# Kernel tuning notes

Measured on AMD Instinct MI355X. Metric: run time of the kernel, lower is better.

## Reference

```python
import jax, jax.numpy as jnp
import numpy as np
import math

C = 512
NUM_HEADS = 4
GROUPS = 32  # group_count(512, 32)
EPS = 1e-5


def group_norm(x, gamma, beta):
    # x: [b, c, h, w]; normalize over (c//GROUPS, h, w) per group
    b, c, h, w = x.shape
    xg = x.reshape(b, GROUPS, -1)
    mu = jnp.mean(xg, axis=-1, keepdims=True)
    var = jnp.var(xg, axis=-1, keepdims=True)
    xn = ((xg - mu) * jax.lax.rsqrt(var + EPS)).reshape(b, c, h, w)
    return xn * gamma[None, :, None, None] + beta[None, :, None, None]


def setup_inputs() -> dict:
    key = jax.random.key(0)
    ks = jax.random.split(key, 5)
    b, h, w = 2, 64, 64
    x = jax.random.normal(ks[0], (b, C, h, w), dtype=jnp.float32)
    gn_w = jnp.ones((C,), dtype=jnp.float32)
    gn_b = jnp.zeros((C,), dtype=jnp.float32)
    s_qkv = 1.0 / math.sqrt(C)
    w_qkv = jax.random.uniform(ks[1], (3 * C, C), jnp.float32, -s_qkv, s_qkv)
    b_qkv = jax.random.uniform(ks[2], (3 * C,), jnp.float32, -s_qkv, s_qkv)
    w_proj = jax.random.uniform(ks[3], (C, C), jnp.float32, -s_qkv, s_qkv)
    b_proj = jax.random.uniform(ks[4], (C,), jnp.float32, -s_qkv, s_qkv)
    return {"x": x, "gn_w": gn_w, "gn_b": gn_b, "w_qkv": w_qkv,
            "b_qkv": b_qkv, "w_proj": w_proj, "b_proj": b_proj}


def reference(x, gn_w, gn_b, w_qkv, b_qkv, w_proj, b_proj):
    b, c, h, w = x.shape
    L = h * w
    nh = NUM_HEADS
    hd = c // nh
    residual = x
    xn = group_norm(x, gn_w, gn_b).reshape(b, c, L)
    # Conv1d with kernel_size=1 == channelwise linear: [b, 3c, L]
    qkv = jnp.einsum('bcl,oc->bol', xn, w_qkv) + b_qkv[None, :, None]
    q, k, v = jnp.split(qkv, 3, axis=1)
    q = q.reshape(b, nh, hd, L)
    k = k.reshape(b, nh, hd, L)
    v = v.reshape(b, nh, hd, L)
    scores = jnp.einsum('bncd,bnce->bnde', q, k) / math.sqrt(hd)
    attn = jax.nn.softmax(scores, axis=-1)
    out = jnp.einsum('bnde,bnce->bncd', attn, v).reshape(b, c, L)
    out = jnp.einsum('bcl,oc->bol', out, w_proj) + b_proj[None, :, None]
    return out.reshape(b, c, h, w) + residual
```

## Files before the change

kernel.cpp:

```cpp
#include <hip/hip_runtime.h>
#include <math.h>

typedef __bf16 bf16;
typedef __bf16 bf16x8 __attribute__((ext_vector_type(8)));
typedef __bf16 bf16x4 __attribute__((ext_vector_type(4)));
typedef float f32x4 __attribute__((ext_vector_type(4)));

#define QSCALE (0.08838834764831845f * 1.4426950408889634f)

__device__ __forceinline__ void gll16(const bf16* g, bf16* l) {
    __builtin_amdgcn_global_load_lds((const __attribute__((address_space(1))) void*)g,
                                     (__attribute__((address_space(3))) void*)l, 16, 0, 0);
}

__global__ void k_pre(const float* __restrict__ wqkv, const float* __restrict__ wproj,
                      const float* __restrict__ x,
                      bf16* __restrict__ wqkv_b, bf16* __restrict__ wproj_b,
                      float* __restrict__ part) {
    int blk = blockIdx.x;
    if (blk < 1024) {
        int i = blk * 256 + threadIdx.x;
        const int n1 = (1536 * 512) / 4;
        float4 v;
        bf16* dst;
        if (i < n1) { v = ((const float4*)wqkv)[i];      dst = wqkv_b + (size_t)i * 4; }
        else        { v = ((const float4*)wproj)[i - n1]; dst = wproj_b + (size_t)(i - n1) * 4; }
        bf16x4 o;
        o[0] = (bf16)v.x; o[1] = (bf16)v.y; o[2] = (bf16)v.z; o[3] = (bf16)v.w;
        *(bf16x4*)dst = o;
        return;
    }
    int b2 = blk - 1024;
    int grp = b2 >> 2, p = b2 & 3;
    const float4* src = (const float4*)(x + (size_t)grp * 65536 + (size_t)p * 16384);
    float s = 0.f, ss = 0.f;
    for (int it = 0; it < 16; ++it) {
        float4 v = src[threadIdx.x + it * 256];
        s  += v.x + v.y + v.z + v.w;
        ss += v.x * v.x + v.y * v.y + v.z * v.z + v.w * v.w;
    }
    for (int off = 32; off; off >>= 1) { s += __shfl_down(s, off); ss += __shfl_down(ss, off); }
    __shared__ float rs[4], rss[4];
    int wave = threadIdx.x >> 6;
    if ((threadIdx.x & 63) == 0) { rs[wave] = s; rss[wave] = ss; }
    __syncthreads();
    if (threadIdx.x == 0) {
        part[(grp * 4 + p) * 2]     = rs[0] + rs[1] + rs[2] + rs[3];
        part[(grp * 4 + p) * 2 + 1] = rss[0] + rss[1] + rss[2] + rss[3];
    }
}

__global__ __launch_bounds__(256) void k_gn_norm_t(const float* __restrict__ x, const float* __restrict__ gw,
                                                   const float* __restrict__ gb, const float* __restrict__ part,
                                                   bf16* __restrict__ xn_t) {
    __shared__ float sX[64 * 69];
    __shared__ float sMean[4], sRstd[4];
    int b = blockIdx.z, c0 = blockIdx.y * 64, l0 = blockIdx.x * 64;
    int t = threadIdx.x;
    if (t < 4) {
        int g = b * 32 + (c0 >> 4) + t;
        float S = 0.f, SS = 0.f;
        for (int p = 0; p < 4; ++p) { S += part[(g * 4 + p) * 2]; SS += part[(g * 4 + p) * 2 + 1]; }
        float mean = S * (1.f / 65536.f);
        float var  = SS * (1.f / 65536.f) - mean * mean;
        sMean[t] = mean;
        sRstd[t] = rsqrtf(var + 1e-5f);
    }
    __syncthreads();
    int cr = t >> 4, lq = t & 15;
    const float* xp = x + ((size_t)(b * 512 + c0)) * 4096 + l0;
    for (int i = 0; i < 4; ++i) {
        int c = cr + i * 16;
        int cg = c0 + c;
        float mean = sMean[c >> 4], rstd = sRstd[c >> 4];
        float ga = gw[cg] * rstd;
        float be = gb[cg] - mean * ga;
        float4 v = *(const float4*)(xp + (size_t)c * 4096 + lq * 4);
        float* d = &sX[c * 69 + lq * 4];
        d[0] = v.x * ga + be; d[1] = v.y * ga + be; d[2] = v.z * ga + be; d[3] = v.w * ga + be;
    }
    __syncthreads();
    int lr = t >> 3, cp = t & 7;
    bf16* dst = xn_t + ((size_t)b * 4096 + l0) * 512 + c0;
    for (int i = 0; i < 2; ++i) {
        int l = lr + i * 32;
        bf16x8 o;
        for (int j = 0; j < 8; ++j) o[j] = (bf16)sX[(cp * 8 + j) * 69 + l];
        *(bf16x8*)(dst + (size_t)l * 512 + cp * 8) = o;
    }
}

__global__ __launch_bounds__(256, 3) void k_gemm_qkv(
    const bf16* __restrict__ A, const bf16* __restrict__ W, const float* __restrict__ bias,
    bf16* __restrict__ qkT, bf16* __restrict__ vb) {
    __shared__ bf16 smem[17408];
    int linear = blockIdx.x + 12 * blockIdx.y + 384 * blockIdx.z;
    int swz = (linear & 7) * 96 + (linear >> 3);
    int n0 = (swz % 12) * 128;
    int m0 = ((swz / 12) % 32) * 128;
    int bz = swz / 384;
    int tid = threadIdx.x, lane = tid & 63, wave = tid >> 6;
    int lo = lane & 15, quad = lane >> 4;
    int lr = lane >> 3, ls = lane & 7;
    int mw = (wave >> 1) * 64, nw = (wave & 1) * 64;
    const bf16* aptr[4]; int adst[4];
    const bf16* bptr[4]; int bdst[4];
    for (int i = 0; i < 4; ++i) {
        int r0 = wave * 32 + i * 8;
        int row = r0 + lr;
        aptr[i] = A + (size_t)bz * (4096 * 512) + (size_t)(m0 + row) * 512 + ((ls ^ (row & 7)) * 8);
        adst[i] = r0 * 64;
        bptr[i] = W + (size_t)(n0 + row) * 512 + ((ls ^ (row & 7)) * 8);
        bdst[i] = 8192 + r0 * 64;
    }
    f32x4 acc[4][4] = {};
    for (int step = 0; step < 8; ++step) {
        __syncthreads();
        for (int i = 0; i < 4; ++i) {
            gll16(aptr[i], &smem[adst[i]]); aptr[i] += 64;
            gll16(bptr[i], &smem[bdst[i]]); bptr[i] += 64;
        }
        __syncthreads();
        const bf16* sA = smem;
        const bf16* sB = smem + 8192;
        for (int kk = 0; kk < 2; ++kk) {
            bf16x8 af[4], bfr[4];
            int sw = ((kk * 4 + quad) ^ (lo & 7)) * 8;
            for (int t = 0; t < 4; ++t) af[t]  = *(const bf16x8*)&sA[(mw + t * 16 + lo) * 64 + sw];
            for (int t = 0; t < 4; ++t) bfr[t] = *(const bf16x8*)&sB[(nw + t * 16 + lo) * 64 + sw];
            for (int mt = 0; mt < 4; ++mt)
                for (int nt = 0; nt < 4; ++nt)
                    acc[mt][nt] = __builtin_amdgcn_mfma_f32_16x16x32_bf16(af[mt], bfr[nt], acc[mt][nt], 0, 0, 0);
        }
    }
    __syncthreads();
    bf16* sT = smem;
    bool isv = (n0 >= 1024);
    float sc = (n0 < 512) ? QSCALE : 1.f;
    for (int mt = 0; mt < 4; ++mt)
        for (int nt = 0; nt < 4; ++nt) {
            int c = nw + nt * 16 + lo;
            float bv = bias[n0 + c];
            for (int r = 0; r < 4; ++r) {
                int l = mw + mt * 16 + quad * 4 + r;
                float v = (acc[mt][nt][r] + bv) * sc;
                if (isv) sT[c * 136 + l] = (bf16)v;
                else     sT[l * 136 + c] = (bf16)v;
            }
        }
    __syncthreads();
    int row = tid >> 1, hh = tid & 1;
    if (isv) {
        bf16* dst = vb + (size_t)bz * (512 * 4096) + (size_t)(n0 - 1024 + row) * 4096 + m0;
        for (int j = 0; j < 8; ++j) {
            int ch = hh + j * 2;
            *(bf16x8*)(dst + ch * 8) = *(const bf16x8*)&sT[row * 136 + ch * 8];
        }
    } else {
        bf16* dst = qkT + (size_t)bz * (4096 * 1024) + (size_t)(m0 + row) * 1024 + n0;
        for (int j = 0; j < 8; ++j) {
            int ch = hh + j * 2;
            *(bf16x8*)(dst + ch * 8) = *(const bf16x8*)&sT[row * 136 + ch * 8];
        }
    }
}

__global__ __launch_bounds__(256, 3) void k_gemm_proj(
    const bf16* __restrict__ W, const bf16* __restrict__ Bm,
    const float* __restrict__ bias_m,
    float* __restrict__ outf, const float* __restrict__ resid) {
    constexpr int BUF = (64 + 128) * 64;
    __shared__ bf16 smem[2 * BUF];
    int bz = blockIdx.z;
    int m0 = blockIdx.y * 64, n0 = blockIdx.x * 128;
    int tid = threadIdx.x, lane = tid & 63, wave = tid >> 6;
    int lo = lane & 15, quad = lane >> 4;
    int lr = lane >> 3, ls = lane & 7;
    int mw = (wave >> 1) * 32, nw = (wave & 1) * 64;
    const bf16* aptr[2]; int adst[2];
    for (int i = 0; i < 2; ++i) {
        int r0 = wave * 16 + i * 8;
        int row = r0 + lr;
        aptr[i] = W + (size_t)(m0 + row) * 512 + ((ls ^ (row & 7)) * 8);
        adst[i] = r0 * 64;
    }
    const bf16* bptr[4]; int bdst[4];
    for (int i = 0; i < 4; ++i) {
        int r0 = wave * 32 + i * 8;
        int row = r0 + lr;
        bptr[i] = Bm + (size_t)bz * (4096 * 512) + (size_t)(n0 + row) * 512 + ((ls ^ (row & 7)) * 8);
        bdst[i] = 64 * 64 + r0 * 64;
    }
    f32x4 acc[2][4] = {};
    for (int i = 0; i < 2; ++i) { gll16(aptr[i], &smem[adst[i]]); aptr[i] += 64; }
    for (int i = 0; i < 4; ++i) { gll16(bptr[i], &smem[bdst[i]]); bptr[i] += 64; }
    for (int step = 0; step < 8; ++step) {
        int cur = step & 1;
        __syncthreads();
        if (step < 7) {
            bf16* nb = &smem[(cur ^ 1) * BUF];
            for (int i = 0; i < 2; ++i) { gll16(aptr[i], nb + adst[i]); aptr[i] += 64; }
            for (int i = 0; i < 4; ++i) { gll16(bptr[i], nb + bdst[i]); bptr[i] += 64; }
        }
        const bf16* sA = &smem[cur * BUF];
        const bf16* sB = sA + 64 * 64;
        for (int kk = 0; kk < 2; ++kk) {
            bf16x8 af[2], bfr[4];
            int sw = ((kk * 4 + quad) ^ (lo & 7)) * 8;
            for (int t = 0; t < 2; ++t) af[t]  = *(const bf16x8*)&sA[(mw + t * 16 + lo) * 64 + sw];
            for (int t = 0; t < 4; ++t) bfr[t] = *(const bf16x8*)&sB[(nw + t * 16 + lo) * 64 + sw];
            for (int mt = 0; mt < 2; ++mt)
                for (int nt = 0; nt < 4; ++nt)
                    acc[mt][nt] = __builtin_amdgcn_mfma_f32_16x16x32_bf16(af[mt], bfr[nt], acc[mt][nt], 0, 0, 0);
        }
    }
    for (int mt = 0; mt < 2; ++mt) {
        int rowb = m0 + mw + mt * 16 + quad * 4;
        for (int nt = 0; nt < 4; ++nt) {
            int col = n0 + nw + nt * 16 + lo;
            for (int r = 0; r < 4; ++r) {
                int row = rowb + r;
                size_t idx = (size_t)bz * (512 * 4096) + (size_t)row * 4096 + col;
                outf[idx] = acc[mt][nt][r] + bias_m[row] + resid[idx];
            }
        }
    }
}

__global__ __launch_bounds__(512, 2) void k_attn(const bf16* __restrict__ qkT, const bf16* __restrict__ vmat,
                                                 bf16* __restrict__ attnT) {
    __shared__ __align__(16) char smem[104448];
    bf16* sE = (bf16*)smem;
    float* sStat = (float*)(smem + 102400);
    int bidx = blockIdx.x;
    int bh = bidx & 7;
    int bb = bh >> 2, h = bh & 3;
    int l0 = (bidx >> 3) * 128;
    int tid = threadIdx.x, lane = tid & 63, wave = tid >> 6;
    int lo = lane & 15, quad = lane >> 4;
    int a = wave & 3, b2 = wave >> 2;
    int lr16 = lane >> 4, ls16 = lane & 15;
    int lr8 = lane >> 3, ls8 = lane & 7;
    const bf16* qbase = qkT + ((size_t)bb * 4096 + l0) * 1024 + h * 128;
    const bf16* kbase = qkT + (size_t)bb * 4096 * 1024 + 512 + h * 128;
    const bf16* vbase = vmat + (size_t)(bb * 512 + h * 128) * 4096;
    for (int i = 0; i < 4; ++i) {
        int r0 = wave * 16 + i * 4;
        int row = r0 + lr16;
        gll16(qbase + (size_t)row * 1024 + ((ls16 ^ (row & 15)) * 8), sE + r0 * 128);
    }
    __syncthreads();
    bf16x8 qf[2][4];
    for (int nt = 0; nt < 2; ++nt) {
        int row = a * 32 + nt * 16 + lo;
        for (int kk = 0; kk < 4; ++kk)
            qf[nt][kk] = *(const bf16x8*)&sE[row * 128 + (((kk * 4 + quad) ^ lo) * 8)];
    }
    __syncthreads();
    const bf16* kptr[2]; int kdst[2];
    const bf16* vptr[2]; int vdst[2];
    for (int i = 0; i < 2; ++i) {
        int r0 = wave * 8 + i * 4;
        int row = r0 + lr16;
        kptr[i] = kbase + (size_t)row * 1024 + ((ls16 ^ (row & 15)) * 8);
        kdst[i] = r0 * 128;
        int s0 = wave * 16 + i * 8;
        int srow = s0 + lr8;
        vptr[i] = vbase + (size_t)srow * 4096 + ((ls8 ^ (srow & 7)) * 8);
        vdst[i] = s0 * 64;
    }
    bf16* sPe = (bf16*)(smem + 65536) + wave * 1280;
    float l_r[2];
    l_r[0] = l_r[1] = 0.f;
    f32x4 oacc[8][2] = {};
    for (int i = 0; i < 2; ++i) { gll16(kptr[i], sE + kdst[i]); kptr[i] += (size_t)64 * 1024; }
    for (int i = 0; i < 2; ++i) { gll16(vptr[i], sE + 16384 + vdst[i]); vptr[i] += 64; }
    for (int it = 0; it < 64; ++it) {
        int cur = it & 1;
        __syncthreads();
        if (it < 63) {
            bf16* nk = sE + (cur ^ 1) * 8192;
            bf16* nv = sE + 16384 + (cur ^ 1) * 8192;
            for (int i = 0; i < 2; ++i) { gll16(kptr[i], nk + kdst[i]); kptr[i] += (size_t)64 * 1024; }
            for (int i = 0; i < 2; ++i) { gll16(vptr[i], nv + vdst[i]); vptr[i] += 64; }
        }
        const bf16* sK = sE + cur * 8192;
        const bf16* sV = sE + 16384 + cur * 8192;
        f32x4 s[2][2];
        for (int mt = 0; mt < 2; ++mt) {
            int krow = b2 * 32 + mt * 16 + lo;
            bf16x8 kf[4];
            for (int kk = 0; kk < 4; ++kk)
                kf[kk] = *(const bf16x8*)&sK[krow * 128 + (((kk * 4 + quad) ^ lo) * 8)];
            for (int nt = 0; nt < 2; ++nt) {
                f32x4 acc = {};
                for (int kk = 0; kk < 4; ++kk)
                    acc = __builtin_amdgcn_mfma_f32_16x16x32_bf16(kf[kk], qf[nt][kk], acc, 0, 0, 0);
                s[mt][nt] = acc;
            }
        }
        for (int nt = 0; nt < 2; ++nt) {
            float sm = 0.f;
            for (int mt = 0; mt < 2; ++mt) {
                bf16x4 pk;
                for (int r = 0; r < 4; ++r) {
                    float pv = __builtin_amdgcn_exp2f(s[mt][nt][r]);
                    sm += pv;
                    pk[r] = (bf16)pv;
                }
                *(bf16x4*)&sPe[(nt * 16 + lo) * 40 + mt * 16 + quad * 4] = pk;
            }
            l_r[nt] += sm;
        }
        bf16x8 pf[2];
        for (int nt = 0; nt < 2; ++nt)
            pf[nt] = *(const bf16x8*)&sPe[(nt * 16 + lo) * 40 + quad * 8];
        for (int mt2 = 0; mt2 < 8; ++mt2) {
            bf16x8 vf = *(const bf16x8*)&sV[(mt2 * 16 + lo) * 64 + (((b2 * 4 + quad) ^ (lo & 7)) * 8)];
            for (int nt = 0; nt < 2; ++nt)
                oacc[mt2][nt] = __builtin_amdgcn_mfma_f32_16x16x32_bf16(vf, pf[nt], oacc[mt2][nt], 0, 0, 0);
        }
    }
    for (int nt = 0; nt < 2; ++nt) {
        l_r[nt] += __shfl_xor(l_r[nt], 16);
        l_r[nt] += __shfl_xor(l_r[nt], 32);
    }
    __syncthreads();
    if (quad == 0) {
        for (int nt = 0; nt < 2; ++nt) {
            int qb = a * 32 + nt * 16 + lo;
            sStat[qb * 2 + b2] = l_r[nt];
        }
    }
    __syncthreads();
    float inv[2];
    for (int nt = 0; nt < 2; ++nt) {
        int qb = a * 32 + nt * 16 + lo;
        inv[nt] = 1.f / (sStat[qb * 2] + sStat[qb * 2 + 1]);
    }
    float* sOm = (float*)smem;
    bf16* sOut = (bf16*)(smem + 67584);
    if (b2 == 1) {
        for (int mt2 = 0; mt2 < 8; ++mt2)
            for (int nt = 0; nt < 2; ++nt)
                for (int r = 0; r < 4; ++r) {
                    int vc = mt2 * 16 + quad * 4 + r;
                    sOm[a * 4224 + vc * 33 + nt * 16 + lo] = oacc[mt2][nt][r];
                }
    }
    __syncthreads();
    if (b2 == 0) {
        for (int mt2 = 0; mt2 < 8; ++mt2)
            for (int nt = 0; nt < 2; ++nt)
                for (int r = 0; r < 4; ++r) {
                    int vc = mt2 * 16 + quad * 4 + r;
                    float v = (oacc[mt2][nt][r] + sOm[a * 4224 + vc * 33 + nt * 16 + lo]) * inv[nt];
                    sOut[(a * 32 + nt * 16 + lo) * 136 + vc] = (bf16)v;
                }
    }
    __syncthreads();
    bf16* dst = attnT + ((size_t)bb * 4096 + l0) * 512 + h * 128;
    for (int i = 0; i < 4; ++i) {
        int row = (tid >> 4) + i * 32;
        int chunk = tid & 15;
        bf16x8 v = *(const bf16x8*)&sOut[row * 136 + chunk * 8];
        *(bf16x8*)(dst + (size_t)row * 512 + chunk * 8) = v;
    }
}

extern "C" void kernel_launch(void* const* d_in, const int* in_sizes, int n_in,
                              void* d_out, int out_size, void* d_ws, size_t ws_size,
                              hipStream_t stream) {
    const float* x      = (const float*)d_in[0];
    const float* gn_w   = (const float*)d_in[1];
    const float* gn_b   = (const float*)d_in[2];
    const float* w_qkv  = (const float*)d_in[3];
    const float* b_qkv  = (const float*)d_in[4];
    const float* w_proj = (const float*)d_in[5];
    const float* b_proj = (const float*)d_in[6];
    float* out = (float*)d_out;
    char* ws = (char*)d_ws;
    bf16* wqkv_b  = (bf16*)(ws + 0);
    bf16* wproj_b = (bf16*)(ws + 1572864);
    bf16* xn_t    = (bf16*)(ws + 2097152);
    bf16* qkT     = (bf16*)(ws + 10485760);
    bf16* vb      = (bf16*)(ws + 27262976);
    bf16* attnT   = (bf16*)(ws + 35651584);
    float* part   = (float*)(ws + 44040192);

    k_pre<<<1280, 256, 0, stream>>>(w_qkv, w_proj, x, wqkv_b, wproj_b, part);
    k_gn_norm_t<<<dim3(64, 8, 2), 256, 0, stream>>>(x, gn_w, gn_b, part, xn_t);
    k_gemm_qkv<<<dim3(12, 32, 2), 256, 0, stream>>>(xn_t, wqkv_b, b_qkv, qkT, vb);
    k_attn<<<256, 512, 0, stream>>>(qkT, vb, attnT);
    k_gemm_proj<<<dim3(32, 8, 2), 256, 0, stream>>>(wproj_b, attnT, b_proj, out, x);
}
```

Measured before the change: 186.8 us.

## Restructure attention tiles: 128-key blocks, 64-query waves, 4-way key split

The attention kernel now processes 128 keys per iteration (32 iterations instead of 64), with each wave holding 64 query rows and the key dimension split four ways across waves. The larger per-wave tile is meant to raise MFMA work per LDS load and halve barrier count, and s_setprio hints are added around the MFMA bursts. In exchange it uses 160KB of shared memory, which likely limits occupancy to one block per CU despite launch bounds of 2, raises register pressure (oacc grows to 8x4), and needs a multi-stage cross-wave reduction at the end.

```diff
diff --git a/kernel.cpp b/kernel.cpp
--- a/kernel.cpp
+++ b/kernel.cpp
@@ -229,133 +229,152 @@
 
 __global__ __launch_bounds__(512, 2) void k_attn(const bf16* __restrict__ qkT, const bf16* __restrict__ vmat,
                                                  bf16* __restrict__ attnT) {
-    __shared__ __align__(16) char smem[104448];
+    __shared__ __align__(16) char smem[163840];
     bf16* sE = (bf16*)smem;
-    float* sStat = (float*)(smem + 102400);
     int bidx = blockIdx.x;
     int bh = bidx & 7;
     int bb = bh >> 2, h = bh & 3;
     int l0 = (bidx >> 3) * 128;
     int tid = threadIdx.x, lane = tid & 63, wave = tid >> 6;
     int lo = lane & 15, quad = lane >> 4;
-    int a = wave & 3, b2 = wave >> 2;
-    int lr16 = lane >> 4, ls16 = lane & 15;
-    int lr8 = lane >> 3, ls8 = lane & 7;
+    int a = wave & 1, b2 = wave >> 1;
     const bf16* qbase = qkT + ((size_t)bb * 4096 + l0) * 1024 + h * 128;
     const bf16* kbase = qkT + (size_t)bb * 4096 * 1024 + 512 + h * 128;
     const bf16* vbase = vmat + (size_t)(bb * 512 + h * 128) * 4096;
     for (int i = 0; i < 4; ++i) {
         int r0 = wave * 16 + i * 4;
-        int row = r0 + lr16;
-        gll16(qbase + (size_t)row * 1024 + ((ls16 ^ (row & 15)) * 8), sE + r0 * 128);
-    }
-    __syncthreads();
-    bf16x8 qf[2][4];
-    for (int nt = 0; nt < 2; ++nt) {
-        int row = a * 32 + nt * 16 + lo;
+        int row = r0 + quad;
+        gll16(qbase + (size_t)row * 1024 + ((lo ^ (row & 15)) * 8), sE + r0 * 128);
+    }
+    __syncthreads();
+    bf16x8 qf[4][4];
+    for (int nt = 0; nt < 4; ++nt) {
+        int row = a * 64 + nt * 16 + lo;
         for (int kk = 0; kk < 4; ++kk)
             qf[nt][kk] = *(const bf16x8*)&sE[row * 128 + (((kk * 4 + quad) ^ lo) * 8)];
     }
     __syncthreads();
-    const bf16* kptr[2]; int kdst[2];
-    const bf16* vptr[2]; int vdst[2];
-    for (int i = 0; i < 2; ++i) {
-        int r0 = wave * 8 + i * 4;
-        int row = r0 + lr16;
-        kptr[i] = kbase + (size_t)row * 1024 + ((ls16 ^ (row & 15)) * 8);
+    const bf16* kp[4]; int kdst[4];
+    const bf16* vp[4]; int vdst[4];
+    for (int i = 0; i < 4; ++i) {
+        int r0 = wave * 16 + i * 4;
+        int row = r0 + quad;
+        kp[i] = kbase + (size_t)row * 1024 + ((lo ^ (row & 15)) * 8);
         kdst[i] = r0 * 128;
-        int s0 = wave * 16 + i * 8;
-        int srow = s0 + lr8;
-        vptr[i] = vbase + (size_t)srow * 4096 + ((ls8 ^ (srow & 7)) * 8);
-        vdst[i] = s0 * 64;
-    }
-    bf16* sPe = (bf16*)(smem + 65536) + wave * 1280;
-    float l_r[2];
-    l_r[0] = l_r[1] = 0.f;
-    f32x4 oacc[8][2] = {};
-    for (int i = 0; i < 2; ++i) { gll16(kptr[i], sE + kdst[i]); kptr[i] += (size_t)64 * 1024; }
-    for (int i = 0; i < 2; ++i) { gll16(vptr[i], sE + 16384 + vdst[i]); vptr[i] += 64; }
-    for (int it = 0; it < 64; ++it) {
+        vp[i] = vbase + (size_t)row * 4096 + ((lo ^ (row & 15)) * 8);
+        vdst[i] = 32768 + r0 * 128;
+    }
+    char* sPb = smem + 131072 + a * 16384;
+    float l_r[4] = {};
+    f32x4 oacc[8][4] = {};
+    for (int i = 0; i < 4; ++i) { gll16(kp[i], sE + kdst[i]); kp[i] += 131072; }
+    for (int i = 0; i < 4; ++i) { gll16(vp[i], sE + vdst[i]); vp[i] += 128; }
+    for (int it = 0; it < 32; ++it) {
         int cur = it & 1;
         __syncthreads();
-        if (it < 63) {
-            bf16* nk = sE + (cur ^ 1) * 8192;
-            bf16* nv = sE + 16384 + (cur ^ 1) * 8192;
-            for (int i = 0; i < 2; ++i) { gll16(kptr[i], nk + kdst[i]); kptr[i] += (size_t)64 * 1024; }
-            for (int i = 0; i < 2; ++i) { gll16(vptr[i], nv + vdst[i]); vptr[i] += 64; }
-        }
-        const bf16* sK = sE + cur * 8192;
-        const bf16* sV = sE + 16384 + cur * 8192;
-        f32x4 s[2][2];
+        if (it < 31) {
+            int nb = (cur ^ 1) * 16384;
+            for (int i = 0; i < 4; ++i) { gll16(kp[i], sE + nb + kdst[i]); kp[i] += 131072; }
+            for (int i = 0; i < 4; ++i) { gll16(vp[i], sE + nb + vdst[i]); vp[i] += 128; }
+        }
+        const bf16* sK = sE + cur * 16384;
+        const bf16* sV = sE + 32768 + cur * 16384;
+        bf16x8 kf[2][4];
         for (int mt = 0; mt < 2; ++mt) {
             int krow = b2 * 32 + mt * 16 + lo;
-            bf16x8 kf[4];
             for (int kk = 0; kk < 4; ++kk)
-                kf[kk] = *(const bf16x8*)&sK[krow * 128 + (((kk * 4 + quad) ^ lo) * 8)];
-            for (int nt = 0; nt < 2; ++nt) {
-                f32x4 acc = {};
-                for (int kk = 0; kk < 4; ++kk)
-                    acc = __builtin_amdgcn_mfma_f32_16x16x32_bf16(kf[kk], qf[nt][kk], acc, 0, 0, 0);
-                s[mt][nt] = acc;
-            }
-        }
-        for (int nt = 0; nt < 2; ++nt) {
+                kf[mt][kk] = *(const bf16x8*)&sK[krow * 128 + (((kk * 4 + quad) ^ lo) * 8)];
+        }
+        for (int nt = 0; nt < 4; ++nt) {
+            f32x4 s0 = {}, s1 = {};
+            __builtin_amdgcn_s_setprio(1);
+            for (int kk = 0; kk < 4; ++kk)
+                s0 = __builtin_amdgcn_mfma_f32_16x16x32_bf16(kf[0][kk], qf[nt][kk], s0, 0, 0, 0);
+            for (int kk = 0; kk < 4; ++kk)
+                s1 = __builtin_amdgcn_mfma_f32_16x16x32_bf16(kf[1][kk], qf[nt][kk], s1, 0, 0, 0);
+            __builtin_amdgcn_s_setprio(0);
             float sm = 0.f;
-            for (int mt = 0; mt < 2; ++mt) {
+            int qrow = (nt * 16 + lo) * 256;
+            {
                 bf16x4 pk;
                 for (int r = 0; r < 4; ++r) {
-                    float pv = __builtin_amdgcn_exp2f(s[mt][nt][r]);
-                    sm += pv;
-                    pk[r] = (bf16)pv;
+                    float pv = __builtin_amdgcn_exp2f(s0[r]);
+                    sm += pv; pk[r] = (bf16)pv;
                 }
-                *(bf16x4*)&sPe[(nt * 16 + lo) * 40 + mt * 16 + quad * 4] = pk;
+                *(bf16x4*)&sPb[qrow + ((((b2 << 2) + (quad >> 1)) ^ lo) << 4) + ((quad & 1) << 3)] = pk;
+            }
+            {
+                bf16x4 pk;
+                for (int r = 0; r < 4; ++r) {
+                    float pv = __builtin_amdgcn_exp2f(s1[r]);
+                    sm += pv; pk[r] = (bf16)pv;
+                }
+                *(bf16x4*)&sPb[qrow + ((((b2 << 2) + 2 + (quad >> 1)) ^ lo) << 4) + ((quad & 1) << 3)] = pk;
             }
             l_r[nt] += sm;
         }
-        bf16x8 pf[2];
-        for (int nt = 0; nt < 2; ++nt)
-            pf[nt] = *(const bf16x8*)&sPe[(nt * 16 + lo) * 40 + quad * 8];
+        bf16x8 pf[4];
+        for (int nt = 0; nt < 4; ++nt)
+            pf[nt] = *(const bf16x8*)&sPb[(nt * 16 + lo) * 256 + ((((b2 << 2) + quad) ^ lo) << 4)];
+        __builtin_amdgcn_s_setprio(1);
         for (int mt2 = 0; mt2 < 8; ++mt2) {
-            bf16x8 vf = *(const bf16x8*)&sV[(mt2 * 16 + lo) * 64 + (((b2 * 4 + quad) ^ (lo & 7)) * 8)];
-            for (int nt = 0; nt < 2; ++nt)
+            bf16x8 vf = *(const bf16x8*)&sV[(mt2 * 16 + lo) * 128 + ((((b2 << 2) + quad) ^ lo) * 8)];
+            for (int nt = 0; nt < 4; ++nt)
                 oacc[mt2][nt] = __builtin_amdgcn_mfma_f32_16x16x32_bf16(vf, pf[nt], oacc[mt2][nt], 0, 0, 0);
         }
-    }
-    for (int nt = 0; nt < 2; ++nt) {
+        __builtin_amdgcn_s_setprio(0);
+    }
+    for (int nt = 0; nt < 4; ++nt) {
         l_r[nt] += __shfl_xor(l_r[nt], 16);
         l_r[nt] += __shfl_xor(l_r[nt], 32);
     }
     __syncthreads();
-    if (quad == 0) {
-        for (int nt = 0; nt < 2; ++nt) {
-            int qb = a * 32 + nt * 16 + lo;
-            sStat[qb * 2 + b2] = l_r[nt];
-        }
-    }
-    __syncthreads();
-    float inv[2];
-    for (int nt = 0; nt < 2; ++nt) {
-        int qb = a * 32 + nt * 16 + lo;
-        inv[nt] = 1.f / (sStat[qb * 2] + sStat[qb * 2 + 1]);
-    }
-    float* sOm = (float*)smem;
-    bf16* sOut = (bf16*)(smem + 67584);
-    if (b2 == 1) {
+    float* sStat = (float*)(smem + 139264);
+    if (quad == 0)
+        for (int nt = 0; nt < 4; ++nt)
+            sStat[(a * 64 + nt * 16 + lo) * 4 + b2] = l_r[nt];
+    __syncthreads();
+    float* sOmA = (float*)smem;
+    float* sOmB = (float*)(smem + 69632);
+    float inv[4];
+    if (b2 == 0)
+        for (int nt = 0; nt < 4; ++nt) {
+            const float* st = &sStat[(a * 64 + nt * 16 + lo) * 4];
+            inv[nt] = 1.f / (st[0] + st[1] + st[2] + st[3]);
+        }
+    if (b2 == 1 || b2 == 3) {
+        float* dm = (b2 == 1 ? sOmA : sOmB) + a * 8704;
         for (int mt2 = 0; mt2 < 8; ++mt2)
-            for (int nt = 0; nt < 2; ++nt)
+            for (int nt = 0; nt < 4; ++nt)
+                for (int r = 0; r < 4; ++r)
+                    dm[(mt2 * 16 + quad * 4 + r) * 68 + nt * 16 + lo] = oacc[mt2][nt][r];
+    }
+    __syncthreads();
+    if (b2 == 0 || b2 == 2) {
+        const float* sm2 = (b2 == 0 ? sOmA : sOmB) + a * 8704;
+        for (int mt2 = 0; mt2 < 8; ++mt2)
+            for (int nt = 0; nt < 4; ++nt)
+                for (int r = 0; r < 4; ++r)
+                    oacc[mt2][nt][r] += sm2[(mt2 * 16 + quad * 4 + r) * 68 + nt * 16 + lo];
+    }
+    __syncthreads();
+    if (b2 == 2) {
+        float* dm = sOmA + a * 8704;
+        for (int mt2 = 0; mt2 < 8; ++mt2)
+            for (int nt = 0; nt < 4; ++nt)
+                for (int r = 0; r < 4; ++r)
+                    dm[(mt2 * 16 + quad * 4 + r) * 68 + nt * 16 + lo] = oacc[mt2][nt][r];
+    }
+    __syncthreads();
+    bf16* sOut = (bf16*)(smem + 69632);
+    if (b2 == 0) {
+        const float* sm2 = sOmA + a * 8704;
+        for (int mt2 = 0; mt2 < 8; ++mt2)
+            for (int nt = 0; nt < 4; ++nt)
                 for (int r = 0; r < 4; ++r) {
                     int vc = mt2 * 16 + quad * 4 + r;
-                    sOm[a * 4224 + vc * 33 + nt * 16 + lo] = oacc[mt2][nt][r];
-                }
-    }
-    __syncthreads();
-    if (b2 == 0) {
-        for (int mt2 = 0; mt2 < 8; ++mt2)
-            for (int nt = 0; nt < 2; ++nt)
-                for (int r = 0; r < 4; ++r) {
-                    int vc = mt2 * 16 + quad * 4 + r;
-                    float v = (oacc[mt2][nt][r] + sOm[a * 4224 + vc * 33 + nt * 16 + lo]) * inv[nt];
-                    sOut[(a * 32 + nt * 16 + lo) * 136 + vc] = (bf16)v;
+                    float v = (oacc[mt2][nt][r] + sm2[vc * 68 + nt * 16 + lo]) * inv[nt];
+                    sOut[(a * 64 + nt * 16 + lo) * 136 + vc] = (bf16)v;
                 }
     }
     __syncthreads();
```

New measurement: 256.3 us. 37.2% more time.

## Double the attention key tile to 128 and add MFMA priority hints

Applied to the files above, without the earlier changes.

The attention kernel now processes 128 keys per iteration instead of 64. That halves the loop trip count and the number of block barriers, and K/V tiles are loaded with four async LDS loads per thread. Shared memory grows to 160KB, the P-tile layout is changed to a 128-byte swizzled row per query, and s_setprio brackets are placed around the MFMA sections. The cost is much larger LDS use, which with launch_bounds(512,2) can limit residency to one block per CU, plus more registers held per iteration.

```diff
diff --git a/kernel.cpp b/kernel.cpp
--- a/kernel.cpp
+++ b/kernel.cpp
@@ -229,9 +229,8 @@
 
 __global__ __launch_bounds__(512, 2) void k_attn(const bf16* __restrict__ qkT, const bf16* __restrict__ vmat,
                                                  bf16* __restrict__ attnT) {
-    __shared__ __align__(16) char smem[104448];
+    __shared__ __align__(16) char smem[163840];
     bf16* sE = (bf16*)smem;
-    float* sStat = (float*)(smem + 102400);
     int bidx = blockIdx.x;
     int bh = bidx & 7;
     int bb = bh >> 2, h = bh & 3;
@@ -239,15 +238,13 @@
     int tid = threadIdx.x, lane = tid & 63, wave = tid >> 6;
     int lo = lane & 15, quad = lane >> 4;
     int a = wave & 3, b2 = wave >> 2;
-    int lr16 = lane >> 4, ls16 = lane & 15;
-    int lr8 = lane >> 3, ls8 = lane & 7;
     const bf16* qbase = qkT + ((size_t)bb * 4096 + l0) * 1024 + h * 128;
     const bf16* kbase = qkT + (size_t)bb * 4096 * 1024 + 512 + h * 128;
     const bf16* vbase = vmat + (size_t)(bb * 512 + h * 128) * 4096;
     for (int i = 0; i < 4; ++i) {
         int r0 = wave * 16 + i * 4;
-        int row = r0 + lr16;
-        gll16(qbase + (size_t)row * 1024 + ((ls16 ^ (row & 15)) * 8), sE + r0 * 128);
+        int row = r0 + quad;
+        gll16(qbase + (size_t)row * 1024 + ((lo ^ (row & 15)) * 8), sE + r0 * 128);
     }
     __syncthreads();
     bf16x8 qf[2][4];
@@ -257,75 +254,74 @@
             qf[nt][kk] = *(const bf16x8*)&sE[row * 128 + (((kk * 4 + quad) ^ lo) * 8)];
     }
     __syncthreads();
-    const bf16* kptr[2]; int kdst[2];
-    const bf16* vptr[2]; int vdst[2];
-    for (int i = 0; i < 2; ++i) {
-        int r0 = wave * 8 + i * 4;
-        int row = r0 + lr16;
-        kptr[i] = kbase + (size_t)row * 1024 + ((ls16 ^ (row & 15)) * 8);
+    const bf16* kp[4]; int kdst[4];
+    const bf16* vp[4]; int vdst[4];
+    for (int i = 0; i < 4; ++i) {
+        int r0 = wave * 16 + i * 4;
+        int row = r0 + quad;
+        kp[i] = kbase + (size_t)row * 1024 + ((lo ^ (row & 15)) * 8);
         kdst[i] = r0 * 128;
-        int s0 = wave * 16 + i * 8;
-        int srow = s0 + lr8;
-        vptr[i] = vbase + (size_t)srow * 4096 + ((ls8 ^ (srow & 7)) * 8);
-        vdst[i] = s0 * 64;
-    }
-    bf16* sPe = (bf16*)(smem + 65536) + wave * 1280;
+        vp[i] = vbase + (size_t)row * 4096 + ((lo ^ (row & 15)) * 8);
+        vdst[i] = 32768 + r0 * 128;
+    }
+    char* sPb = smem + 131072 + wave * 4096;
+    int swz8 = lo & 7;
     float l_r[2];
     l_r[0] = l_r[1] = 0.f;
     f32x4 oacc[8][2] = {};
-    for (int i = 0; i < 2; ++i) { gll16(kptr[i], sE + kdst[i]); kptr[i] += (size_t)64 * 1024; }
-    for (int i = 0; i < 2; ++i) { gll16(vptr[i], sE + 16384 + vdst[i]); vptr[i] += 64; }
-    for (int it = 0; it < 64; ++it) {
+    for (int i = 0; i < 4; ++i) { gll16(kp[i], sE + kdst[i]); kp[i] += (size_t)128 * 1024; }
+    for (int i = 0; i < 4; ++i) { gll16(vp[i], sE + vdst[i]); vp[i] += 128; }
+    for (int it = 0; it < 32; ++it) {
         int cur = it & 1;
         __syncthreads();
-        if (it < 63) {
-            bf16* nk = sE + (cur ^ 1) * 8192;
-            bf16* nv = sE + 16384 + (cur ^ 1) * 8192;
-            for (int i = 0; i < 2; ++i) { gll16(kptr[i], nk + kdst[i]); kptr[i] += (size_t)64 * 1024; }
-            for (int i = 0; i < 2; ++i) { gll16(vptr[i], nv + vdst[i]); vptr[i] += 64; }
-        }
-        const bf16* sK = sE + cur * 8192;
-        const bf16* sV = sE + 16384 + cur * 8192;
-        f32x4 s[2][2];
-        for (int mt = 0; mt < 2; ++mt) {
-            int krow = b2 * 32 + mt * 16 + lo;
-            bf16x8 kf[4];
-            for (int kk = 0; kk < 4; ++kk)
-                kf[kk] = *(const bf16x8*)&sK[krow * 128 + (((kk * 4 + quad) ^ lo) * 8)];
-            for (int nt = 0; nt < 2; ++nt) {
-                f32x4 acc = {};
-                for (int kk = 0; kk < 4; ++kk)
-                    acc = __builtin_amdgcn_mfma_f32_16x16x32_bf16(kf[kk], qf[nt][kk], acc, 0, 0, 0);
-                s[mt][nt] = acc;
+        if (it < 31) {
+            int nb = (cur ^ 1) * 16384;
+            for (int i = 0; i < 4; ++i) { gll16(kp[i], sE + nb + kdst[i]); kp[i] += (size_t)128 * 1024; }
+            for (int i = 0; i < 4; ++i) { gll16(vp[i], sE + nb + vdst[i]); vp[i] += 128; }
+        }
+        const bf16* sK = sE + cur * 16384;
+        const bf16* sV = sE + 32768 + cur * 16384;
+        for (int mt = 0; mt < 4; ++mt) {
+            int krow = b2 * 64 + mt * 16 + lo;
+            f32x4 s0 = {}, s1 = {};
+            __builtin_amdgcn_s_setprio(1);
+            for (int kk = 0; kk < 4; ++kk) {
+                bf16x8 kf = *(const bf16x8*)&sK[krow * 128 + (((kk * 4 + quad) ^ lo) * 8)];
+                s0 = __builtin_amdgcn_mfma_f32_16x16x32_bf16(kf, qf[0][kk], s0, 0, 0, 0);
+                s1 = __builtin_amdgcn_mfma_f32_16x16x32_bf16(kf, qf[1][kk], s1, 0, 0, 0);
             }
-        }
-        for (int nt = 0; nt < 2; ++nt) {
-            float sm = 0.f;
-            for (int mt = 0; mt < 2; ++mt) {
-                bf16x4 pk;
-                for (int r = 0; r < 4; ++r) {
-                    float pv = __builtin_amdgcn_exp2f(s[mt][nt][r]);
-                    sm += pv;
-                    pk[r] = (bf16)pv;
-                }
-                *(bf16x4*)&sPe[(nt * 16 + lo) * 40 + mt * 16 + quad * 4] = pk;
+            __builtin_amdgcn_s_setprio(0);
+            int cw = (((2 * mt + (quad >> 1)) ^ swz8) << 4) + ((quad & 1) << 3);
+            float sm0 = 0.f, sm1 = 0.f;
+            bf16x4 pk;
+            for (int r = 0; r < 4; ++r) { float pv = __builtin_amdgcn_exp2f(s0[r]); sm0 += pv; pk[r] = (bf16)pv; }
+            *(bf16x4*)&sPb[lo * 128 + cw] = pk;
+            for (int r = 0; r < 4; ++r) { float pv = __builtin_amdgcn_exp2f(s1[r]); sm1 += pv; pk[r] = (bf16)pv; }
+            *(bf16x4*)&sPb[(16 + lo) * 128 + cw] = pk;
+            l_r[0] += sm0;
+            l_r[1] += sm1;
+        }
+        bf16x8 pf[2][2];
+        for (int nt = 0; nt < 2; ++nt)
+            for (int kk = 0; kk < 2; ++kk)
+                pf[nt][kk] = *(const bf16x8*)&sPb[(nt * 16 + lo) * 128 + (((kk * 4 + quad) ^ swz8) << 4)];
+        __builtin_amdgcn_s_setprio(1);
+        for (int mt2 = 0; mt2 < 8; ++mt2) {
+            int vrow = mt2 * 16 + lo;
+            for (int kk = 0; kk < 2; ++kk) {
+                bf16x8 vf = *(const bf16x8*)&sV[vrow * 128 + (((b2 * 8 + kk * 4 + quad) ^ lo) * 8)];
+                oacc[mt2][0] = __builtin_amdgcn_mfma_f32_16x16x32_bf16(vf, pf[0][kk], oacc[mt2][0], 0, 0, 0);
+                oacc[mt2][1] = __builtin_amdgcn_mfma_f32_16x16x32_bf16(vf, pf[1][kk], oacc[mt2][1], 0, 0, 0);
             }
-            l_r[nt] += sm;
-        }
-        bf16x8 pf[2];
-        for (int nt = 0; nt < 2; ++nt)
-            pf[nt] = *(const bf16x8*)&sPe[(nt * 16 + lo) * 40 + quad * 8];
-        for (int mt2 = 0; mt2 < 8; ++mt2) {
-            bf16x8 vf = *(const bf16x8*)&sV[(mt2 * 16 + lo) * 64 + (((b2 * 4 + quad) ^ (lo & 7)) * 8)];
-            for (int nt = 0; nt < 2; ++nt)
-                oacc[mt2][nt] = __builtin_amdgcn_mfma_f32_16x16x32_bf16(vf, pf[nt], oacc[mt2][nt], 0, 0, 0);
-        }
+        }
+        __builtin_amdgcn_s_setprio(0);
     }
     for (int nt = 0; nt < 2; ++nt) {
         l_r[nt] += __shfl_xor(l_r[nt], 16);
         l_r[nt] += __shfl_xor(l_r[nt], 32);
     }
     __syncthreads();
+    float* sStat = (float*)(smem + 139264);
     if (quad == 0) {
         for (int nt = 0; nt < 2; ++nt) {
             int qb = a * 32 + nt * 16 + lo;
```

After: 188.9 us. No clear change (+1.1%).
